# Optimization experiments

Hardware: AMD Instinct MI355X
Metric: run time of the kernel (lower is better)

## Reference

```python
import jax, jax.numpy as jnp
import numpy as np
from jax import lax

K_SIZE = 3
STRIDE = 1
PAD = 1
BN_EPS = 1e-5


def _unfold(x, k, stride, pad):
    # x: [B, C, H, W] -> patches [B, L, C*k*k] with torch.unfold feature
    # ordering (channel-major: feat = c*k*k + i*k + j), L = oH*oW
    B, C, H, W = x.shape
    xp = jnp.pad(x, ((0, 0), (0, 0), (pad, pad), (pad, pad)))
    oH = (H + 2 * pad - k) // stride + 1
    oW = (W + 2 * pad - k) // stride + 1
    views = []
    for i in range(k):
        for j in range(k):
            views.append(xp[:, :, i:i + oH * stride:stride, j:j + oW * stride:stride])
    p = jnp.stack(views, axis=0)            # [k*k, B, C, oH, oW]
    p = p.transpose(1, 3, 4, 2, 0)          # [B, oH, oW, C, k*k]
    return p.reshape(B, oH * oW, C * k * k), oH, oW


def _nearest_l1(flat, cents):
    # Online nearest-centroid search under L1, avoids [N, K] x D blowup.
    # flat: [N, D], cents: [K, D] -> int32 indices [N] (first min on ties,
    # matching torch argmin)
    N = flat.shape[0]
    init = (jnp.full((N,), jnp.inf, flat.dtype), jnp.zeros((N,), jnp.int32))
    ks = jnp.arange(cents.shape[0], dtype=jnp.int32)

    def body(carry, kc):
        kidx, c = kc
        d = jnp.abs(flat - c).sum(-1)       # [N]
        bd, bi = carry
        better = d < bd
        return (jnp.where(better, d, bd), jnp.where(better, kidx, bi)), None

    (_, best_idx), _ = lax.scan(body, init, (ks, cents))
    return best_idx


def setup_inputs() -> dict:
    key = jax.random.key(0)
    ks = jax.random.split(key, 5)
    B, Cin, H, W = 8, 64, 56, 56
    K, D, Cout = 256, Cin * K_SIZE * K_SIZE, 128
    return {
        "x": jax.random.normal(ks[0], (B, Cin, H, W), jnp.float32),
        "centroids": jax.random.normal(ks[1], (K, D), jnp.float32),
        "residual_centroids": jax.random.normal(ks[2], (K, D), jnp.float32),
        "dot_centroids": jax.random.normal(ks[3], (K, Cout), jnp.float32),
        "dot_residual_centroids": jax.random.normal(ks[4], (K, Cout), jnp.float32),
        "bn_gamma": jnp.ones((Cout,), jnp.float32),
        "bn_beta": jnp.zeros((Cout,), jnp.float32),
    }


def reference(x, centroids, residual_centroids, dot_centroids,
              dot_residual_centroids, bn_gamma, bn_beta):
    B = x.shape[0]
    Cout = dot_centroids.shape[1]
    patches, oH, oW = _unfold(x, K_SIZE, STRIDE, PAD)   # [B, L, D]
    L, D = patches.shape[1], patches.shape[2]
    flat = patches.reshape(B * L, D)

    # Stage 1: nearest centroid (L1)
    idx1 = _nearest_l1(flat, centroids)                  # [B*L]
    residuals = flat - centroids[idx1]                   # [B*L, D]
    # Stage 2: nearest residual centroid (L1)
    idx2 = _nearest_l1(residuals, residual_centroids)    # [B*L]

    # LUT gather + sum
    out_vals = dot_centroids[idx1] + dot_residual_centroids[idx2]  # [B*L, Cout]
    out = out_vals.reshape(B, L, Cout).transpose(0, 2, 1).reshape(B, Cout, oH, oW)

    # BatchNorm2d (training mode: biased batch statistics)
    mean = out.mean(axis=(0, 2, 3), keepdims=True)
    var = ((out - mean) ** 2).mean(axis=(0, 2, 3), keepdims=True)
    out = (out - mean) * lax.rsqrt(var + BN_EPS)
    out = out * bn_gamma[None, :, None, None] + bn_beta[None, :, None, None]
    return out
```

## Files before the change

### kernel.cpp

```cpp
#include <hip/hip_runtime.h>
#include <stdint.h>

#define NP 25088
#define DD 576
#define KC 256

__global__ __launch_bounds__(256) void unfold_kernel(const float* __restrict__ x,
                                                     float* __restrict__ P) {
  const int n0 = blockIdx.x * 16;
#pragma unroll 1
  for (int rr = 0; rr < 36; ++rr) {
    const unsigned idx = rr * 256 + threadIdx.x;
    const int n = n0 + (int)(idx / 576u);
    const int d = (int)(idx % 576u);
    const int c = d / 9, r = d % 9;
    const int di = r / 3 - 1, dj = r % 3 - 1;
    const int b = n / 3136, hw = n % 3136;
    const int h = hw / 56 + di, w = hw % 56 + dj;
    float v = 0.0f;
    if (h >= 0 && h < 56 && w >= 0 && w < 56)
      v = x[(((size_t)b * 64 + c) * 56 + h) * 56 + w];
    P[(size_t)n * DD + d] = v;
  }
}

#define STEP(mm, ACC) do {                                          \
    const float* Ar_ = ap + (size_t)(mm) * DD;                      \
    const float4 a0 = *(const float4*)(Ar_);                        \
    const float4 a1 = *(const float4*)(Ar_ + 4);                    \
    const float4 a2 = *(const float4*)(Ar_ + 8);                    \
    const float4 a3 = *(const float4*)(Ar_ + 12);                   \
    const float s_ =                                                \
      ((((fabsf(a0.x - vb0.x) + fabsf(a0.y - vb0.y)) +              \
         (fabsf(a0.z - vb0.z) + fabsf(a0.w - vb0.w))) +             \
        ((fabsf(a1.x - vb1.x) + fabsf(a1.y - vb1.y)) +              \
         (fabsf(a1.z - vb1.z) + fabsf(a1.w - vb1.w)))) +            \
       (((fabsf(a2.x - vb2.x) + fabsf(a2.y - vb2.y)) +              \
         (fabsf(a2.z - vb2.z) + fabsf(a2.w - vb2.w))) +             \
        ((fabsf(a3.x - vb3.x) + fabsf(a3.y - vb3.y)) +              \
         (fabsf(a3.z - vb3.z) + fabsf(a3.w - vb3.w)))));            \
    ACC += s_;                                                      \
  } while (0)

#define REDUCE(mm, V) do {                                          \
    float bd_ = (V); int bk_ = tid;                                 \
    _Pragma("unroll")                                               \
    for (int off_ = 1; off_ < 64; off_ <<= 1) {                     \
      const float od_ = __shfl_xor(bd_, off_, 64);                  \
      const int ok_ = __shfl_xor(bk_, off_, 64);                    \
      if (od_ < bd_ || (od_ == bd_ && ok_ < bk_)) { bd_ = od_; bk_ = ok_; } \
    }                                                               \
    if (lane == 0) { sd[wv][mm] = bd_; si[wv][mm] = bk_; }          \
  } while (0)

__global__ __launch_bounds__(256, 4) void nearest_kernel(const float* __restrict__ A,
                                                         const float* __restrict__ C,
                                                         int* __restrict__ idx_out) {
  __shared__ float sd[4][16];
  __shared__ int si[4][16];

  const int tid = threadIdx.x;
  const int lane = tid & 63, wv = tid >> 6;
  const int m0 = blockIdx.x * 16;

  const float* ap = A + (size_t)m0 * DD;
  const float* bp = C + (size_t)tid * DD;

  float4 acc0, acc1, acc2, acc3;
  acc0 = acc1 = acc2 = acc3 = make_float4(0.f, 0.f, 0.f, 0.f);

#pragma unroll 2
  for (int ch = 0; ch < 36; ++ch) {
    const float4 vb0 = *(const float4*)(bp);
    const float4 vb1 = *(const float4*)(bp + 4);
    const float4 vb2 = *(const float4*)(bp + 8);
    const float4 vb3 = *(const float4*)(bp + 12);
    STEP(0,  acc0.x); STEP(1,  acc0.y); STEP(2,  acc0.z); STEP(3,  acc0.w);
    STEP(4,  acc1.x); STEP(5,  acc1.y); STEP(6,  acc1.z); STEP(7,  acc1.w);
    STEP(8,  acc2.x); STEP(9,  acc2.y); STEP(10, acc2.z); STEP(11, acc2.w);
    STEP(12, acc3.x); STEP(13, acc3.y); STEP(14, acc3.z); STEP(15, acc3.w);
    ap += 16; bp += 16;
  }

  REDUCE(0,  acc0.x); REDUCE(1,  acc0.y); REDUCE(2,  acc0.z); REDUCE(3,  acc0.w);
  REDUCE(4,  acc1.x); REDUCE(5,  acc1.y); REDUCE(6,  acc1.z); REDUCE(7,  acc1.w);
  REDUCE(8,  acc2.x); REDUCE(9,  acc2.y); REDUCE(10, acc2.z); REDUCE(11, acc2.w);
  REDUCE(12, acc3.x); REDUCE(13, acc3.y); REDUCE(14, acc3.z); REDUCE(15, acc3.w);

  __syncthreads();
  if (tid < 16) {
    float bd = sd[0][tid];
    int bk = si[0][tid];
#pragma unroll
    for (int w = 1; w < 4; ++w) {
      const float od = sd[w][tid];
      if (od < bd) { bd = od; bk = si[w][tid]; }
    }
    idx_out[m0 + tid] = bk;
  }
}

__global__ __launch_bounds__(256) void resid_kernel(float* __restrict__ P,
                                                    const float* __restrict__ C1,
                                                    const int* __restrict__ idx1) {
  const int n0 = blockIdx.x * 16;
#pragma unroll 1
  for (int rr = 0; rr < 9; ++rr) {
    const unsigned q = rr * 256 + threadIdx.x;
    const int n = n0 + (int)(q / 144u);
    const int dq = (int)(q % 144u);
    const int k = idx1[n];
    float4* pp = (float4*)(P + (size_t)n * DD + dq * 4);
    const float4 pv = *pp;
    const float4 cv = *(const float4*)(C1 + (size_t)k * DD + dq * 4);
    *pp = make_float4(pv.x - cv.x, pv.y - cv.y, pv.z - cv.z, pv.w - cv.w);
  }
}

__global__ __launch_bounds__(256) void stats_kernel(const int* __restrict__ idx1,
                                                    const int* __restrict__ idx2,
                                                    const float* __restrict__ dotc,
                                                    const float* __restrict__ dotrc,
                                                    float* __restrict__ gsum,
                                                    float* __restrict__ gsq) {
  __shared__ float ssum[4][128], ssq[4][128];
  const int tid = threadIdx.x, lane = tid & 63, wv = tid >> 6;
  const int wid = blockIdx.x * 4 + wv;
  float s0 = 0.f, s1 = 0.f, q0 = 0.f, q1 = 0.f;
  for (int n = wid; n < NP; n += 512) {
    const int k1 = idx1[n], k2 = idx2[n];
    const float2 u = ((const float2*)(dotc + (size_t)k1 * 128))[lane];
    const float2 v = ((const float2*)(dotrc + (size_t)k2 * 128))[lane];
    const float x0 = u.x + v.x, x1 = u.y + v.y;
    s0 += x0; s1 += x1; q0 += x0 * x0; q1 += x1 * x1;
  }
  ssum[wv][lane * 2] = s0; ssum[wv][lane * 2 + 1] = s1;
  ssq[wv][lane * 2] = q0;  ssq[wv][lane * 2 + 1] = q1;
  __syncthreads();
  if (tid < 128) {
    const float s = ssum[0][tid] + ssum[1][tid] + ssum[2][tid] + ssum[3][tid];
    const float q = ssq[0][tid] + ssq[1][tid] + ssq[2][tid] + ssq[3][tid];
    atomicAdd(&gsum[tid], s);
    atomicAdd(&gsq[tid], q);
  }
}

__global__ void finalize_kernel(const float* __restrict__ gsum,
                                const float* __restrict__ gsq,
                                const float* __restrict__ gamma,
                                const float* __restrict__ beta,
                                float* __restrict__ scalev,
                                float* __restrict__ shiftv) {
  const int c = threadIdx.x;
  const float mean = gsum[c] * (1.0f / NP);
  const float var = gsq[c] * (1.0f / NP) - mean * mean;
  const float inv = rsqrtf(var + 1e-5f);
  const float sc = gamma[c] * inv;
  scalev[c] = sc;
  shiftv[c] = beta[c] - mean * sc;
}

__global__ __launch_bounds__(256) void output_kernel(const int* __restrict__ idx1,
                                                     const int* __restrict__ idx2,
                                                     const float* __restrict__ dotc,
                                                     const float* __restrict__ dotrc,
                                                     const float* __restrict__ scalev,
                                                     const float* __restrict__ shiftv,
                                                     float* __restrict__ out) {
  __shared__ float vals[64][128];
  const int tid = threadIdx.x, lane = tid & 63, wv = tid >> 6;
  const int blk = blockIdx.x;
  const int b = blk / 49, hw0 = (blk % 49) * 64;
  const int n0 = b * 3136 + hw0;
  const float sc0 = scalev[lane * 2], sc1 = scalev[lane * 2 + 1];
  const float sh0 = shiftv[lane * 2], sh1 = shiftv[lane * 2 + 1];
  for (int t = 0; t < 16; ++t) {
    const int nn = wv * 16 + t;
    const int n = n0 + nn;
    const int k1 = idx1[n], k2 = idx2[n];
    const float2 u = ((const float2*)(dotc + (size_t)k1 * 128))[lane];
    const float2 v = ((const float2*)(dotrc + (size_t)k2 * 128))[lane];
    *(float2*)&vals[nn][lane * 2] =
        make_float2(sc0 * (u.x + v.x) + sh0, sc1 * (u.y + v.y) + sh1);
  }
  __syncthreads();
  const int c = tid >> 1, half = tid & 1;
  float* op = out + ((size_t)b * 128 + c) * 3136 + hw0 + half * 32;
#pragma unroll
  for (int i = 0; i < 32; i += 4) {
    float4 w4;
    w4.x = vals[half * 32 + i + 0][c];
    w4.y = vals[half * 32 + i + 1][c];
    w4.z = vals[half * 32 + i + 2][c];
    w4.w = vals[half * 32 + i + 3][c];
    *(float4*)(op + i) = w4;
  }
}

extern "C" void kernel_launch(void* const* d_in, const int* in_sizes, int n_in,
                              void* d_out, int out_size, void* d_ws, size_t ws_size,
                              hipStream_t stream) {
  const float* x     = (const float*)d_in[0];
  const float* cent  = (const float*)d_in[1];
  const float* rcent = (const float*)d_in[2];
  const float* dotc  = (const float*)d_in[3];
  const float* dotrc = (const float*)d_in[4];
  const float* gamma = (const float*)d_in[5];
  const float* beta  = (const float*)d_in[6];
  float* out = (float*)d_out;

  float* P   = (float*)d_ws;
  int* idx1  = (int*)(P + (size_t)NP * DD);
  int* idx2  = idx1 + NP;
  float* gsum   = (float*)(idx2 + NP);
  float* gsq    = gsum + 128;
  float* scalev = gsq + 128;
  float* shiftv = scalev + 128;

  unfold_kernel<<<1568, 256, 0, stream>>>(x, P);
  nearest_kernel<<<1568, 256, 0, stream>>>(P, cent, idx1);
  resid_kernel<<<1568, 256, 0, stream>>>(P, cent, idx1);
  nearest_kernel<<<1568, 256, 0, stream>>>(P, rcent, idx2);
  hipMemsetAsync(gsum, 0, 256 * sizeof(float), stream);
  stats_kernel<<<128, 256, 0, stream>>>(idx1, idx2, dotc, dotrc, gsum, gsq);
  finalize_kernel<<<1, 128, 0, stream>>>(gsum, gsq, gamma, beta, scalev, shiftv);
  output_kernel<<<392, 256, 0, stream>>>(idx1, idx2, dotc, dotrc, scalev, shiftv, out);
}
```

Measured before the change: 624.9 us.

## Stage patch rows in LDS and software-prefetch centroid chunks in nearest kernel

The nearest-centroid kernel now copies each block's 16 patch rows into shared memory in two halves of 288 floats, so all 256 threads read the shared A values from LDS instead of issuing redundant global or cache loads. Centroid chunks are prefetched one iteration ahead in registers to hide global-load latency. The launch-bounds occupancy hint rises from 4 to 6 blocks per CU, which tightens the register budget and adds about 18KB of LDS per block plus extra barriers.

New measurement: 910.8 us. 45.7% more time.

```diff
diff --git a/kernel.cpp b/kernel.cpp
--- a/kernel.cpp
+++ b/kernel.cpp
@@ -25,11 +25,10 @@
 }
 
 #define STEP(mm, ACC) do {                                          \
-    const float* Ar_ = ap + (size_t)(mm) * DD;                      \
-    const float4 a0 = *(const float4*)(Ar_);                        \
-    const float4 a1 = *(const float4*)(Ar_ + 4);                    \
-    const float4 a2 = *(const float4*)(Ar_ + 8);                    \
-    const float4 a3 = *(const float4*)(Ar_ + 12);                   \
+    const float4 a0 = *(const float4*)&Alds[mm][cb];                \
+    const float4 a1 = *(const float4*)&Alds[mm][cb + 4];            \
+    const float4 a2 = *(const float4*)&Alds[mm][cb + 8];            \
+    const float4 a3 = *(const float4*)&Alds[mm][cb + 12];           \
     const float s_ =                                                \
       ((((fabsf(a0.x - vb0.x) + fabsf(a0.y - vb0.y)) +              \
          (fabsf(a0.z - vb0.z) + fabsf(a0.w - vb0.w))) +             \
@@ -53,9 +52,10 @@
     if (lane == 0) { sd[wv][mm] = bd_; si[wv][mm] = bk_; }          \
   } while (0)
 
-__global__ __launch_bounds__(256, 4) void nearest_kernel(const float* __restrict__ A,
+__global__ __launch_bounds__(256, 6) void nearest_kernel(const float* __restrict__ A,
                                                          const float* __restrict__ C,
                                                          int* __restrict__ idx_out) {
+  __shared__ __align__(16) float Alds[16][288];
   __shared__ float sd[4][16];
   __shared__ int si[4][16];
 
@@ -63,23 +63,41 @@
   const int lane = tid & 63, wv = tid >> 6;
   const int m0 = blockIdx.x * 16;
 
-  const float* ap = A + (size_t)m0 * DD;
   const float* bp = C + (size_t)tid * DD;
 
+  float4 vb0 = *(const float4*)(bp);
+  float4 vb1 = *(const float4*)(bp + 4);
+  float4 vb2 = *(const float4*)(bp + 8);
+  float4 vb3 = *(const float4*)(bp + 12);
   float4 acc0, acc1, acc2, acc3;
   acc0 = acc1 = acc2 = acc3 = make_float4(0.f, 0.f, 0.f, 0.f);
 
-#pragma unroll 2
-  for (int ch = 0; ch < 36; ++ch) {
-    const float4 vb0 = *(const float4*)(bp);
-    const float4 vb1 = *(const float4*)(bp + 4);
-    const float4 vb2 = *(const float4*)(bp + 8);
-    const float4 vb3 = *(const float4*)(bp + 12);
-    STEP(0,  acc0.x); STEP(1,  acc0.y); STEP(2,  acc0.z); STEP(3,  acc0.w);
-    STEP(4,  acc1.x); STEP(5,  acc1.y); STEP(6,  acc1.z); STEP(7,  acc1.w);
-    STEP(8,  acc2.x); STEP(9,  acc2.y); STEP(10, acc2.z); STEP(11, acc2.w);
-    STEP(12, acc3.x); STEP(13, acc3.y); STEP(14, acc3.z); STEP(15, acc3.w);
-    ap += 16; bp += 16;
+#pragma unroll 1
+  for (int half = 0; half < 2; ++half) {
+    __syncthreads();
+#pragma unroll
+    for (int q = tid; q < 1152; q += 256) {
+      const int row = q / 72, col = (q % 72) * 4;
+      *(float4*)&Alds[row][col] =
+          *(const float4*)(A + (size_t)(m0 + row) * DD + half * 288 + col);
+    }
+    __syncthreads();
+#pragma unroll 1
+    for (int ch = 0; ch < 18; ++ch) {
+      const int g = half * 18 + ch;
+      const int pf = (g < 35) ? 16 : 0;
+      const float4 nb0 = *(const float4*)(bp + pf);
+      const float4 nb1 = *(const float4*)(bp + pf + 4);
+      const float4 nb2 = *(const float4*)(bp + pf + 8);
+      const float4 nb3 = *(const float4*)(bp + pf + 12);
+      const int cb = ch * 16;
+      STEP(0,  acc0.x); STEP(1,  acc0.y); STEP(2,  acc0.z); STEP(3,  acc0.w);
+      STEP(4,  acc1.x); STEP(5,  acc1.y); STEP(6,  acc1.z); STEP(7,  acc1.w);
+      STEP(8,  acc2.x); STEP(9,  acc2.y); STEP(10, acc2.z); STEP(11, acc2.w);
+      STEP(12, acc3.x); STEP(13, acc3.y); STEP(14, acc3.z); STEP(15, acc3.w);
+      vb0 = nb0; vb1 = nb1; vb2 = nb2; vb3 = nb3;
+      bp += 16;
+    }
   }
 
   REDUCE(0,  acc0.x); REDUCE(1,  acc0.y); REDUCE(2,  acc0.z); REDUCE(3,  acc0.w);
```
